# Kernel tuning notes

Hardware: AMD Instinct MI355X
Metric: run time of the kernel (lower is better)

## Reference

```python
import jax, jax.numpy as jnp
import numpy as np

N, E, D, H = 50000, 400000, 128, 256


def setup_inputs() -> dict:
    key = jax.random.key(0)
    ks = jax.random.split(key, 16)
    s = 0.02
    inp = {
        "x": jax.random.normal(ks[0], (N, D), dtype=jnp.float32),
        "edge_index": jax.random.randint(ks[1], (2, E), 0, N, dtype=jnp.int64),
        "steps": 1,
        # encoder MLP: Linear(D->H), Linear(H->H), relu after each
        "enc_w1": jax.random.normal(ks[2], (H, D), dtype=jnp.float32) * s,
        "enc_b1": jnp.zeros((H,), dtype=jnp.float32),
        "enc_w2": jax.random.normal(ks[3], (H, H), dtype=jnp.float32) * s,
        "enc_b2": jnp.zeros((H,), dtype=jnp.float32),
        # GeneralConv lin_msg (root_weight=False, bias=True)
        "msg_w": jax.random.normal(ks[4], (H, H), dtype=jnp.float32) * s,
        "msg_b": jnp.zeros((H,), dtype=jnp.float32),
        # decoder MLP: Linear(2H->H) relu, Linear(H->D) tanh
        "dec_w1": jax.random.normal(ks[5], (H, 2 * H), dtype=jnp.float32) * s,
        "dec_b1": jnp.zeros((H,), dtype=jnp.float32),
        "dec_w2": jax.random.normal(ks[6], (D, H), dtype=jnp.float32) * s,
        "dec_b2": jnp.zeros((D,), dtype=jnp.float32),
    }
    return inp


def reference(x, edge_index, steps, enc_w1, enc_b1, enc_w2, enc_b2,
              msg_w, msg_b, dec_w1, dec_b1, dec_w2, dec_b2):
    src = edge_index[0]
    dst = edge_index[1]
    n = x.shape[0]
    for _ in range(steps):  # steps is a small static python int
        # encoder MLP (batch_norm=False, dropout=0, relu + relu)
        h = jax.nn.relu(x @ enc_w1.T + enc_b1)
        h = jax.nn.relu(h @ enc_w2.T + enc_b2)
        # GeneralConv: message = lin_msg(x_j); aggr='add'; no root weight
        # lin_msg is edge-independent -> transform on nodes, then gather/scatter
        m = h @ msg_w.T + msg_b                      # [N, H]
        out = jax.ops.segment_sum(m[src], dst, num_segments=n)  # [N, H]
        # decoder on cat(out, h): relu then tanh
        d = jax.nn.relu(jnp.concatenate([out, h], axis=-1) @ dec_w1.T + dec_b1)
        x = jnp.tanh(d @ dec_w2.T + dec_b2)
    return x
```

## Files before the change

kernel.cpp:

```cpp
#include <hip/hip_runtime.h>
#include <cmath>


typedef __attribute__((ext_vector_type(8))) short  short8;
typedef __attribute__((ext_vector_type(4))) float  f32x4;
typedef __attribute__((ext_vector_type(4))) unsigned short us4;

typedef unsigned short u16;
typedef unsigned int   u32;

static __device__ __forceinline__ u16 f2bf(float f) {
    u32 u = __float_as_uint(f);
    u = (u + 0x7FFFu + ((u >> 16) & 1u)) >> 16;
    return (u16)u;
}
static __device__ __forceinline__ float bf2f(u16 h) {
    return __uint_as_float(((u32)h) << 16);
}

static __device__ __forceinline__ void g2l16(const void* g, void* l) {
    __builtin_amdgcn_global_load_lds(
        (const __attribute__((address_space(1))) u32*)g,
        (__attribute__((address_space(3))) u32*)l, 16, 0, 0);
}

__global__ __launch_bounds__(512, 4) void enc_fused(
    const float* __restrict__ x, const u16* __restrict__ w1,
    const float* __restrict__ b1, const u16* __restrict__ w2,
    const float* __restrict__ b2, const u16* __restrict__ wm,
    const float* __restrict__ bm, u16* __restrict__ hout,
    u16* __restrict__ mout, const int N)
{
    __shared__ u16 hL[8][4][512];

    const int t    = threadIdx.x;
    const int r0   = blockIdx.x * 64;
    const int wave = t >> 6;
    const int lane = t & 63;
    const int n    = lane & 15;
    const int q    = lane >> 4;
    const int wc   = wave * 32;

#pragma unroll
    for (int k = 0; k < 4; k++) {
        const int f   = t * 4 + k * 2048;
        const int row = f >> 7;
        const int col = f & 127;
        const int gr  = min(r0 + row, N - 1);
        const float4 v = *reinterpret_cast<const float4*>(
            x + (size_t)gr * 128 + col);
        us4 o = { f2bf(v.x), f2bf(v.y), f2bf(v.z), f2bf(v.w) };
        const int idx = (((col >> 3) & 3) * 16 + (row & 15)) * 8 + (col & 7);
        *reinterpret_cast<us4*>(&hL[4 + (col >> 5)][row >> 4][idx]) = o;
    }

    f32x4 acc[4][2];
#pragma unroll
    for (int i = 0; i < 4; i++)
#pragma unroll
        for (int j = 0; j < 2; j++) acc[i][j] = (f32x4)0.0f;

    short8 bp[4][2];
#pragma unroll
    for (int c = 0; c < 4; c++)
#pragma unroll
        for (int j = 0; j < 2; j++)
            bp[c][j] = *reinterpret_cast<const short8*>(
                w1 + (size_t)(wc + j * 16 + n) * 128 + c * 32 + q * 8);

    __syncthreads();

#pragma unroll
    for (int c = 0; c < 4; c++) {
        short8 af[4];
#pragma unroll
        for (int i = 0; i < 4; i++)
            af[i] = *reinterpret_cast<const short8*>(
                &hL[4 + c][i][lane * 8]);
#pragma unroll
        for (int i = 0; i < 4; i++)
#pragma unroll
            for (int j = 0; j < 2; j++)
                acc[i][j] = __builtin_amdgcn_mfma_f32_16x16x32_bf16(
                    af[i], bp[c][j], acc[i][j], 0, 0, 0);
    }

#pragma unroll
    for (int c = 0; c < 4; c++)
#pragma unroll
        for (int j = 0; j < 2; j++)
            bp[c][j] = *reinterpret_cast<const short8*>(
                w2 + (size_t)(wc + j * 16 + n) * 256 + c * 32 + q * 8);

    __syncthreads();

    {
        const float bv0 = b1[wc + n];
        const float bv1 = b1[wc + 16 + n];
        const int np = q * 4;
#pragma unroll
        for (int i = 0; i < 4; i++)
#pragma unroll
            for (int reg = 0; reg < 4; reg++) {
#pragma unroll
                for (int j = 0; j < 2; j++) {
                    const float v = fmaxf(acc[i][j][reg] + (j ? bv1 : bv0), 0.0f);
                    const int q2 = j * 2 + (n >> 3);
                    hL[wave][i][(q2 * 16 + np + reg) * 8 + (n & 7)] = f2bf(v);
                }
            }
    }
    __syncthreads();

#pragma unroll
    for (int i = 0; i < 4; i++)
#pragma unroll
        for (int j = 0; j < 2; j++) acc[i][j] = (f32x4)0.0f;
#pragma unroll
    for (int c = 0; c < 8; c++) {
        short8 af[4];
#pragma unroll
        for (int i = 0; i < 4; i++)
            af[i] = *reinterpret_cast<const short8*>(&hL[c][i][lane * 8]);
#pragma unroll
        for (int i = 0; i < 4; i++)
#pragma unroll
            for (int j = 0; j < 2; j++)
                acc[i][j] = __builtin_amdgcn_mfma_f32_16x16x32_bf16(
                    af[i], bp[c & 3][j], acc[i][j], 0, 0, 0);
        if (c < 4) {
#pragma unroll
            for (int j = 0; j < 2; j++)
                bp[c][j] = *reinterpret_cast<const short8*>(
                    w2 + (size_t)(wc + j * 16 + n) * 256 + (c + 4) * 32 + q * 8);
        }
    }

#pragma unroll
    for (int c = 0; c < 4; c++)
#pragma unroll
        for (int j = 0; j < 2; j++)
            bp[c][j] = *reinterpret_cast<const short8*>(
                wm + (size_t)(wc + j * 16 + n) * 256 + c * 32 + q * 8);

    {
        const float bv0 = b2[wc + n];
        const float bv1 = b2[wc + 16 + n];
        const int np = q * 4;
#pragma unroll
        for (int i = 0; i < 4; i++)
#pragma unroll
            for (int reg = 0; reg < 4; reg++) {
                const int row = r0 + i * 16 + q * 4 + reg;
                if (row < N) {
                    hout[(size_t)row * 256 + wc + n] =
                        f2bf(fmaxf(acc[i][0][reg] + bv0, 0.0f));
                    hout[(size_t)row * 256 + wc + 16 + n] =
                        f2bf(fmaxf(acc[i][1][reg] + bv1, 0.0f));
                }
            }
        __syncthreads();
#pragma unroll
        for (int i = 0; i < 4; i++)
#pragma unroll
            for (int reg = 0; reg < 4; reg++) {
#pragma unroll
                for (int j = 0; j < 2; j++) {
                    const float v = fmaxf(acc[i][j][reg] + (j ? bv1 : bv0), 0.0f);
                    const int q2 = j * 2 + (n >> 3);
                    hL[wave][i][(q2 * 16 + np + reg) * 8 + (n & 7)] = f2bf(v);
                }
            }
    }
    __syncthreads();

#pragma unroll
    for (int i = 0; i < 4; i++)
#pragma unroll
        for (int j = 0; j < 2; j++) acc[i][j] = (f32x4)0.0f;
#pragma unroll
    for (int c = 0; c < 8; c++) {
        short8 af[4];
#pragma unroll
        for (int i = 0; i < 4; i++)
            af[i] = *reinterpret_cast<const short8*>(&hL[c][i][lane * 8]);
#pragma unroll
        for (int i = 0; i < 4; i++)
#pragma unroll
            for (int j = 0; j < 2; j++)
                acc[i][j] = __builtin_amdgcn_mfma_f32_16x16x32_bf16(
                    af[i], bp[c & 3][j], acc[i][j], 0, 0, 0);
        if (c < 4) {
#pragma unroll
            for (int j = 0; j < 2; j++)
                bp[c][j] = *reinterpret_cast<const short8*>(
                    wm + (size_t)(wc + j * 16 + n) * 256 + (c + 4) * 32 + q * 8);
        }
    }
    {
        const float bv0 = bm[wc + n];
        const float bv1 = bm[wc + 16 + n];
#pragma unroll
        for (int i = 0; i < 4; i++)
#pragma unroll
            for (int reg = 0; reg < 4; reg++) {
                const int row = r0 + i * 16 + q * 4 + reg;
                if (row < N) {
                    mout[(size_t)row * 256 + wc + n] =
                        f2bf(acc[i][0][reg] + bv0);
                    mout[(size_t)row * 256 + wc + 16 + n] =
                        f2bf(acc[i][1][reg] + bv1);
                }
            }
    }
}

__global__ __launch_bounds__(512, 4) void dec_fused(
    const u16* __restrict__ aggr, const u16* __restrict__ h,
    const u16* __restrict__ wd1, const float* __restrict__ bd1,
    const u16* __restrict__ wd2, const float* __restrict__ bd2,
    float* __restrict__ out, const int N)
{
    __shared__ u16 dL[8][4][512];

    const int t    = threadIdx.x;
    const int r0   = blockIdx.x * 64;
    const int wave = t >> 6;
    const int lane = t & 63;
    const int n    = lane & 15;
    const int q    = lane >> 4;
    const int wc   = wave * 32;

    const int w4   = wave & 3;
    const int sub  = wave >> 2;
    const int srow = min(r0 + w4 * 16 + (lane & 15), N - 1);
    const int kq8  = (lane >> 4) * 8;
    const u16* aptr = aggr + (size_t)srow * 256 + kq8;
    const u16* hptr = h    + (size_t)srow * 256 + kq8;

#define DEC_STAGE(p, buf)                                                   \
    {                                                                       \
        const int c_  = 2 * (p) + sub;                                      \
        const int kc_ = c_ * 32;                                            \
        const u16* sp_ = (kc_ < 256) ? (aptr + kc_) : (hptr + (kc_ - 256)); \
        g2l16(sp_, &dL[(buf) * 2 + sub][w4][0]);                            \
    }

    f32x4 acc[4][2];
#pragma unroll
    for (int i = 0; i < 4; i++)
#pragma unroll
        for (int j = 0; j < 2; j++) acc[i][j] = (f32x4)0.0f;

    DEC_STAGE(0, 0);
    short8 bp[4][2];
#pragma unroll
    for (int c = 0; c < 4; c++)
#pragma unroll
        for (int j = 0; j < 2; j++)
            bp[c][j] = *reinterpret_cast<const short8*>(
                wd1 + (size_t)(wc + j * 16 + n) * 512 + c * 32 + q * 8);
    __syncthreads();

#pragma unroll
    for (int p = 0; p < 8; p++) {
        if (p < 7) DEC_STAGE(p + 1, (p + 1) & 1);
#pragma unroll
        for (int s = 0; s < 2; s++) {
            const int c = 2 * p + s;
            short8 af[4];
#pragma unroll
            for (int i = 0; i < 4; i++)
                af[i] = *reinterpret_cast<const short8*>(
                    &dL[(p & 1) * 2 + s][i][lane * 8]);
#pragma unroll
            for (int i = 0; i < 4; i++)
#pragma unroll
                for (int j = 0; j < 2; j++)
                    acc[i][j] = __builtin_amdgcn_mfma_f32_16x16x32_bf16(
                        af[i], bp[c & 3][j], acc[i][j], 0, 0, 0);
            if (c + 4 < 16) {
#pragma unroll
                for (int j = 0; j < 2; j++)
                    bp[c & 3][j] = *reinterpret_cast<const short8*>(
                        wd1 + (size_t)(wc + j * 16 + n) * 512 +
                        (c + 4) * 32 + q * 8);
            }
        }
        __syncthreads();
    }
#undef DEC_STAGE

    {
        const float bv0 = bd1[wc + n];
        const float bv1 = bd1[wc + 16 + n];
        const int np = q * 4;
#pragma unroll
        for (int i = 0; i < 4; i++)
#pragma unroll
            for (int reg = 0; reg < 4; reg++) {
#pragma unroll
                for (int j = 0; j < 2; j++) {
                    const float v = fmaxf(acc[i][j][reg] + (j ? bv1 : bv0), 0.0f);
                    const int q2 = j * 2 + (n >> 3);
                    dL[wave][i][(q2 * 16 + np + reg) * 8 + (n & 7)] = f2bf(v);
                }
            }
    }

    const int wc2 = wave * 16;
    short8 b2p[4];
#pragma unroll
    for (int c = 0; c < 4; c++)
        b2p[c] = *reinterpret_cast<const short8*>(
            wd2 + (size_t)(wc2 + n) * 256 + c * 32 + q * 8);
    __syncthreads();

    f32x4 acc2[4];
#pragma unroll
    for (int i = 0; i < 4; i++) acc2[i] = (f32x4)0.0f;
#pragma unroll
    for (int c = 0; c < 8; c++) {
        short8 af[4], bf;
#pragma unroll
        for (int i = 0; i < 4; i++)
            af[i] = *reinterpret_cast<const short8*>(&dL[c][i][lane * 8]);
        bf = b2p[c & 3];
#pragma unroll
        for (int i = 0; i < 4; i++)
            acc2[i] = __builtin_amdgcn_mfma_f32_16x16x32_bf16(
                af[i], bf, acc2[i], 0, 0, 0);
        if (c < 4)
            b2p[c] = *reinterpret_cast<const short8*>(
                wd2 + (size_t)(wc2 + n) * 256 + (c + 4) * 32 + q * 8);
    }
    {
        const float bv = bd2[wc2 + n];
#pragma unroll
        for (int i = 0; i < 4; i++)
#pragma unroll
            for (int reg = 0; reg < 4; reg++) {
                const int row = r0 + i * 16 + q * 4 + reg;
                if (row < N)
                    out[(size_t)row * 128 + wc2 + n] = tanhf(acc2[i][reg] + bv);
            }
    }
}

__global__ __launch_bounds__(256) void cvt6_kernel(
    const float* s0, const float* s1, const float* s2, const float* s3,
    const float* s4,
    u16* d0, u16* d1, u16* d2, u16* d3, u16* d4,
    int* __restrict__ zp,
    int n0, int n1, int n2, int n3, int n4, int nz)
{
    const int i = blockIdx.x * 256 + threadIdx.x;
    if (blockIdx.y == 5) {
        if (i < nz) zp[i] = 0;
        return;
    }
    const float* s; u16* d; int nq;
    switch (blockIdx.y) {
        case 0: s = s0; d = d0; nq = n0; break;
        case 1: s = s1; d = d1; nq = n1; break;
        case 2: s = s2; d = d2; nq = n2; break;
        case 3: s = s3; d = d3; nq = n3; break;
        default: s = s4; d = d4; nq = n4; break;
    }
    if (i < nq) {
        const float4 v = reinterpret_cast<const float4*>(s)[i];
        us4 o = { f2bf(v.x), f2bf(v.y), f2bf(v.z), f2bf(v.w) };
        reinterpret_cast<us4*>(d)[i] = o;
    }
}

__global__ __launch_bounds__(256) void fill_kernel(
    const int* __restrict__ ei, int* __restrict__ cursor,
    int* __restrict__ bucket, const int E, const int Nn)
{
    const int e = blockIdx.x * 256 + threadIdx.x;
    if (e < E) {
        const int src = ei[e];
        const int dst = ei[(size_t)E + e];
        if ((unsigned)dst < (unsigned)Nn) {
            const int pos = atomicAdd(&cursor[dst], 1);
            if (pos < 64) bucket[(size_t)dst * 64 + pos] = src;
        }
    }
}

__global__ __launch_bounds__(256) void gather_sum_kernel(
    const u16* __restrict__ m, const int* __restrict__ bucket,
    const int* __restrict__ cursor, u16* __restrict__ outa, const int Nn)
{
    const int wave = (int)((blockIdx.x * 256u + threadIdx.x) >> 6);
    const int lane = threadIdx.x & 63;
    if (wave >= Nn) return;
    const int cnt = min(cursor[wave], 64);
    const int* bl = bucket + (size_t)wave * 64;
    float a0 = 0.f, a1 = 0.f, a2 = 0.f, a3 = 0.f;
    for (int base = 0; base < cnt; base += 8) {
        int sidx[8];
#pragma unroll
        for (int u = 0; u < 8; u++)
            sidx[u] = (base + u < cnt) ? bl[base + u] : -1;
        us4 v[8];
#pragma unroll
        for (int u = 0; u < 8; u++) {
            const int s = ((unsigned)sidx[u] < (unsigned)Nn) ? sidx[u] : 0;
            v[u] = *reinterpret_cast<const us4*>(&m[(size_t)s * 256 + lane * 4]);
        }
#pragma unroll
        for (int u = 0; u < 8; u++) {
            if ((unsigned)sidx[u] < (unsigned)Nn) {
                a0 += bf2f(v[u].x); a1 += bf2f(v[u].y);
                a2 += bf2f(v[u].z); a3 += bf2f(v[u].w);
            }
        }
    }
    us4 o = { f2bf(a0), f2bf(a1), f2bf(a2), f2bf(a3) };
    *reinterpret_cast<us4*>(&outa[(size_t)wave * 256 + lane * 4]) = o;
}

extern "C" void kernel_launch(void* const* d_in, const int* in_sizes, int n_in,
                              void* d_out, int out_size, void* d_ws, size_t ws_size,
                              hipStream_t stream)
{
    const float* x      = (const float*)d_in[0];
    const int*   ei     = (const int*)d_in[1];
    const float* enc_w1 = (const float*)d_in[3];
    const float* enc_b1 = (const float*)d_in[4];
    const float* enc_w2 = (const float*)d_in[5];
    const float* enc_b2 = (const float*)d_in[6];
    const float* msg_w  = (const float*)d_in[7];
    const float* msg_b  = (const float*)d_in[8];
    const float* dec_w1 = (const float*)d_in[9];
    const float* dec_b1 = (const float*)d_in[10];
    const float* dec_w2 = (const float*)d_in[11];
    const float* dec_b2 = (const float*)d_in[12];

    const int N = 50000, D = 128, H = 256;
    const int E = in_sizes[1] / 2;

    u16* h    = (u16*)d_ws;
    u16* m    = h    + (size_t)N * H;
    u16* aggr = m    + (size_t)N * H;
    u16* w1   = aggr + (size_t)N * H;
    u16* w2   = w1 + 256 * 128;
    u16* wm   = w2 + 256 * 256;
    u16* wd1  = wm + 256 * 256;
    u16* wd2  = wd1 + 256 * 512;
    int* cursor = (int*)(wd2 + 128 * 256);
    int* bucket = cursor + N;

    const dim3 blk(256);
    const dim3 blk512(512);
    const int nb64 = (N + 63) / 64;
    const int cvtx = (N + 255) / 256;

    cvt6_kernel<<<dim3(cvtx, 6), blk, 0, stream>>>(
        enc_w1, enc_w2, msg_w, dec_w1, dec_w2,
        w1, w2, wm, wd1, wd2, cursor,
        256 * 128 / 4, 256 * 256 / 4, 256 * 256 / 4,
        256 * 512 / 4, 128 * 256 / 4, N);

    fill_kernel<<<dim3((E + 255) / 256), blk, 0, stream>>>(
        ei, cursor, bucket, E, N);

    enc_fused<<<dim3(nb64), blk512, 0, stream>>>(
        x, w1, enc_b1, w2, enc_b2, wm, msg_b, h, m, N);

    gather_sum_kernel<<<dim3((N * 64 + 255) / 256), blk, 0, stream>>>(
        m, bucket, cursor, aggr, N);

    dec_fused<<<dim3(nb64), blk512, 0, stream>>>(
        aggr, h, wd1, dec_b1, wd2, dec_b2, (float*)d_out, N);
}
```

Measured before the change: 255.0 us.

## Make encoder kernel persistent with register-resident weights and prefetched input tiles

The encoder kernel now launches 256 persistent blocks that loop over 64-row tiles. The w1 and w2 weight fragments are loaded into registers once per block instead of once per tile. The next tile's x rows are prefetched into registers while the current tile computes, overlapping global loads with MFMA work. This raises register pressure (launch bounds lowered to 2 blocks per CU) and cuts the grid to 256 blocks, which may underfill a GPU with many CUs and reduce latency hiding.

```diff
diff --git a/kernel.cpp b/kernel.cpp
--- a/kernel.cpp
+++ b/kernel.cpp
@@ -24,194 +24,214 @@
         (__attribute__((address_space(3))) u32*)l, 16, 0, 0);
 }
 
-__global__ __launch_bounds__(512, 4) void enc_fused(
+__global__ __launch_bounds__(512, 2) void enc_fused(
     const float* __restrict__ x, const u16* __restrict__ w1,
     const float* __restrict__ b1, const u16* __restrict__ w2,
     const float* __restrict__ b2, const u16* __restrict__ wm,
     const float* __restrict__ bm, u16* __restrict__ hout,
-    u16* __restrict__ mout, const int N)
+    u16* __restrict__ mout, const int N, const int ntiles)
 {
     __shared__ u16 hL[8][4][512];
 
     const int t    = threadIdx.x;
-    const int r0   = blockIdx.x * 64;
     const int wave = t >> 6;
     const int lane = t & 63;
     const int n    = lane & 15;
     const int q    = lane >> 4;
     const int wc   = wave * 32;
 
-#pragma unroll
-    for (int k = 0; k < 4; k++) {
-        const int f   = t * 4 + k * 2048;
-        const int row = f >> 7;
-        const int col = f & 127;
-        const int gr  = min(r0 + row, N - 1);
-        const float4 v = *reinterpret_cast<const float4*>(
-            x + (size_t)gr * 128 + col);
-        us4 o = { f2bf(v.x), f2bf(v.y), f2bf(v.z), f2bf(v.w) };
-        const int idx = (((col >> 3) & 3) * 16 + (row & 15)) * 8 + (col & 7);
-        *reinterpret_cast<us4*>(&hL[4 + (col >> 5)][row >> 4][idx]) = o;
-    }
-
-    f32x4 acc[4][2];
-#pragma unroll
-    for (int i = 0; i < 4; i++)
-#pragma unroll
-        for (int j = 0; j < 2; j++) acc[i][j] = (f32x4)0.0f;
-
-    short8 bp[4][2];
+    short8 b1f[4][2];
 #pragma unroll
     for (int c = 0; c < 4; c++)
 #pragma unroll
         for (int j = 0; j < 2; j++)
-            bp[c][j] = *reinterpret_cast<const short8*>(
+            b1f[c][j] = *reinterpret_cast<const short8*>(
                 w1 + (size_t)(wc + j * 16 + n) * 128 + c * 32 + q * 8);
-
-    __syncthreads();
-
-#pragma unroll
-    for (int c = 0; c < 4; c++) {
-        short8 af[4];
-#pragma unroll
-        for (int i = 0; i < 4; i++)
-            af[i] = *reinterpret_cast<const short8*>(
-                &hL[4 + c][i][lane * 8]);
-#pragma unroll
-        for (int i = 0; i < 4; i++)
-#pragma unroll
-            for (int j = 0; j < 2; j++)
-                acc[i][j] = __builtin_amdgcn_mfma_f32_16x16x32_bf16(
-                    af[i], bp[c][j], acc[i][j], 0, 0, 0);
-    }
-
-#pragma unroll
-    for (int c = 0; c < 4; c++)
+    short8 bW[8][2];
+#pragma unroll
+    for (int c = 0; c < 8; c++)
 #pragma unroll
         for (int j = 0; j < 2; j++)
-            bp[c][j] = *reinterpret_cast<const short8*>(
+            bW[c][j] = *reinterpret_cast<const short8*>(
                 w2 + (size_t)(wc + j * 16 + n) * 256 + c * 32 + q * 8);
-
-    __syncthreads();
-
-    {
-        const float bv0 = b1[wc + n];
-        const float bv1 = b1[wc + 16 + n];
-        const int np = q * 4;
-#pragma unroll
-        for (int i = 0; i < 4; i++)
-#pragma unroll
-            for (int reg = 0; reg < 4; reg++) {
-#pragma unroll
-                for (int j = 0; j < 2; j++) {
-                    const float v = fmaxf(acc[i][j][reg] + (j ? bv1 : bv0), 0.0f);
-                    const int q2 = j * 2 + (n >> 3);
-                    hL[wave][i][(q2 * 16 + np + reg) * 8 + (n & 7)] = f2bf(v);
-                }
-            }
-    }
-    __syncthreads();
-
-#pragma unroll
-    for (int i = 0; i < 4; i++)
-#pragma unroll
-        for (int j = 0; j < 2; j++) acc[i][j] = (f32x4)0.0f;
-#pragma unroll
-    for (int c = 0; c < 8; c++) {
-        short8 af[4];
-#pragma unroll
-        for (int i = 0; i < 4; i++)
-            af[i] = *reinterpret_cast<const short8*>(&hL[c][i][lane * 8]);
-#pragma unroll
-        for (int i = 0; i < 4; i++)
-#pragma unroll
-            for (int j = 0; j < 2; j++)
-                acc[i][j] = __builtin_amdgcn_mfma_f32_16x16x32_bf16(
-                    af[i], bp[c & 3][j], acc[i][j], 0, 0, 0);
-        if (c < 4) {
+    const float bv1_0 = b1[wc + n], bv1_1 = b1[wc + 16 + n];
+    const float bv2_0 = b2[wc + n], bv2_1 = b2[wc + 16 + n];
+    const float bvm_0 = bm[wc + n], bvm_1 = bm[wc + 16 + n];
+
+    const int xcol   = (t & 31) * 4;
+    const int xrow0  = t >> 5;
+    const int xchunk = xcol >> 5;
+    const int xidx   = (((xcol >> 3) & 3) * 16 + xrow0) * 8 + (xcol & 7);
+
+    float4 xr[4];
+    int tile = blockIdx.x;
+#pragma unroll
+    for (int kk = 0; kk < 4; kk++) {
+        const int gr = min(tile * 64 + xrow0 + kk * 16, N - 1);
+        xr[kk] = *reinterpret_cast<const float4*>(x + (size_t)gr * 128 + xcol);
+    }
+
+    for (;;) {
+        const int r0 = tile * 64;
+
+#pragma unroll
+        for (int kk = 0; kk < 4; kk++) {
+            us4 o = { f2bf(xr[kk].x), f2bf(xr[kk].y),
+                      f2bf(xr[kk].z), f2bf(xr[kk].w) };
+            *reinterpret_cast<us4*>(&hL[4 + xchunk][kk][xidx]) = o;
+        }
+        __syncthreads();
+
+        const int ntile = tile + 256;
+        if (ntile < ntiles) {
+#pragma unroll
+            for (int kk = 0; kk < 4; kk++) {
+                const int gr = min(ntile * 64 + xrow0 + kk * 16, N - 1);
+                xr[kk] = *reinterpret_cast<const float4*>(
+                    x + (size_t)gr * 128 + xcol);
+            }
+        }
+
+        f32x4 acc[4][2];
+#pragma unroll
+        for (int i = 0; i < 4; i++)
+#pragma unroll
+            for (int j = 0; j < 2; j++) acc[i][j] = (f32x4)0.0f;
+
+#pragma unroll
+        for (int c = 0; c < 4; c++) {
+            short8 af[4];
+#pragma unroll
+            for (int i = 0; i < 4; i++)
+                af[i] = *reinterpret_cast<const short8*>(
+                    &hL[4 + c][i][lane * 8]);
+#pragma unroll
+            for (int i = 0; i < 4; i++)
+#pragma unroll
+                for (int j = 0; j < 2; j++)
+                    acc[i][j] = __builtin_amdgcn_mfma_f32_16x16x32_bf16(
+                        af[i], b1f[c][j], acc[i][j], 0, 0, 0);
+        }
+
+        short8 bp[4][2];
+#pragma unroll
+        for (int c = 0; c < 4; c++)
 #pragma unroll
             for (int j = 0; j < 2; j++)
                 bp[c][j] = *reinterpret_cast<const short8*>(
-                    w2 + (size_t)(wc + j * 16 + n) * 256 + (c + 4) * 32 + q * 8);
-        }
-    }
-
-#pragma unroll
-    for (int c = 0; c < 4; c++)
-#pragma unroll
-        for (int j = 0; j < 2; j++)
-            bp[c][j] = *reinterpret_cast<const short8*>(
-                wm + (size_t)(wc + j * 16 + n) * 256 + c * 32 + q * 8);
-
-    {
-        const float bv0 = b2[wc + n];
-        const float bv1 = b2[wc + 16 + n];
-        const int np = q * 4;
-#pragma unroll
-        for (int i = 0; i < 4; i++)
-#pragma unroll
-            for (int reg = 0; reg < 4; reg++) {
-                const int row = r0 + i * 16 + q * 4 + reg;
-                if (row < N) {
-                    hout[(size_t)row * 256 + wc + n] =
-                        f2bf(fmaxf(acc[i][0][reg] + bv0, 0.0f));
-                    hout[(size_t)row * 256 + wc + 16 + n] =
-                        f2bf(fmaxf(acc[i][1][reg] + bv1, 0.0f));
+                    wm + (size_t)(wc + j * 16 + n) * 256 + c * 32 + q * 8);
+
+        __syncthreads();
+
+        {
+            const int np = q * 4;
+#pragma unroll
+            for (int i = 0; i < 4; i++)
+#pragma unroll
+                for (int reg = 0; reg < 4; reg++) {
+#pragma unroll
+                    for (int j = 0; j < 2; j++) {
+                        const float v = fmaxf(
+                            acc[i][j][reg] + (j ? bv1_1 : bv1_0), 0.0f);
+                        const int q2 = j * 2 + (n >> 3);
+                        hL[wave][i][(q2 * 16 + np + reg) * 8 + (n & 7)] =
+                            f2bf(v);
+                    }
                 }
-            }
-        __syncthreads();
-#pragma unroll
-        for (int i = 0; i < 4; i++)
-#pragma unroll
-            for (int reg = 0; reg < 4; reg++) {
-#pragma unroll
-                for (int j = 0; j < 2; j++) {
-                    const float v = fmaxf(acc[i][j][reg] + (j ? bv1 : bv0), 0.0f);
-                    const int q2 = j * 2 + (n >> 3);
-                    hL[wave][i][(q2 * 16 + np + reg) * 8 + (n & 7)] = f2bf(v);
+        }
+        __syncthreads();
+
+#pragma unroll
+        for (int i = 0; i < 4; i++)
+#pragma unroll
+            for (int j = 0; j < 2; j++) acc[i][j] = (f32x4)0.0f;
+#pragma unroll
+        for (int c = 0; c < 8; c++) {
+            short8 af[4];
+#pragma unroll
+            for (int i = 0; i < 4; i++)
+                af[i] = *reinterpret_cast<const short8*>(&hL[c][i][lane * 8]);
+#pragma unroll
+            for (int i = 0; i < 4; i++)
+#pragma unroll
+                for (int j = 0; j < 2; j++)
+                    acc[i][j] = __builtin_amdgcn_mfma_f32_16x16x32_bf16(
+                        af[i], bW[c][j], acc[i][j], 0, 0, 0);
+        }
+
+        {
+            const int np = q * 4;
+#pragma unroll
+            for (int i = 0; i < 4; i++)
+#pragma unroll
+                for (int reg = 0; reg < 4; reg++) {
+                    const int row = r0 + i * 16 + q * 4 + reg;
+                    if (row < N) {
+                        hout[(size_t)row * 256 + wc + n] =
+                            f2bf(fmaxf(acc[i][0][reg] + bv2_0, 0.0f));
+                        hout[(size_t)row * 256 + wc + 16 + n] =
+                            f2bf(fmaxf(acc[i][1][reg] + bv2_1, 0.0f));
+                    }
                 }
-            }
-    }
-    __syncthreads();
-
-#pragma unroll
-    for (int i = 0; i < 4; i++)
-#pragma unroll
-        for (int j = 0; j < 2; j++) acc[i][j] = (f32x4)0.0f;
-#pragma unroll
-    for (int c = 0; c < 8; c++) {
-        short8 af[4];
-#pragma unroll
-        for (int i = 0; i < 4; i++)
-            af[i] = *reinterpret_cast<const short8*>(&hL[c][i][lane * 8]);
-#pragma unroll
-        for (int i = 0; i < 4; i++)
-#pragma unroll
-            for (int j = 0; j < 2; j++)
-                acc[i][j] = __builtin_amdgcn_mfma_f32_16x16x32_bf16(
-                    af[i], bp[c & 3][j], acc[i][j], 0, 0, 0);
-        if (c < 4) {
-#pragma unroll
-            for (int j = 0; j < 2; j++)
-                bp[c][j] = *reinterpret_cast<const short8*>(
-                    wm + (size_t)(wc + j * 16 + n) * 256 + (c + 4) * 32 + q * 8);
-        }
-    }
-    {
-        const float bv0 = bm[wc + n];
-        const float bv1 = bm[wc + 16 + n];
-#pragma unroll
-        for (int i = 0; i < 4; i++)
-#pragma unroll
-            for (int reg = 0; reg < 4; reg++) {
-                const int row = r0 + i * 16 + q * 4 + reg;
-                if (row < N) {
-                    mout[(size_t)row * 256 + wc + n] =
-                        f2bf(acc[i][0][reg] + bv0);
-                    mout[(size_t)row * 256 + wc + 16 + n] =
-                        f2bf(acc[i][1][reg] + bv1);
+            __syncthreads();
+#pragma unroll
+            for (int i = 0; i < 4; i++)
+#pragma unroll
+                for (int reg = 0; reg < 4; reg++) {
+#pragma unroll
+                    for (int j = 0; j < 2; j++) {
+                        const float v = fmaxf(
+                            acc[i][j][reg] + (j ? bv2_1 : bv2_0), 0.0f);
+                        const int q2 = j * 2 + (n >> 3);
+                        hL[wave][i][(q2 * 16 + np + reg) * 8 + (n & 7)] =
+                            f2bf(v);
+                    }
                 }
-            }
+        }
+        __syncthreads();
+
+#pragma unroll
+        for (int i = 0; i < 4; i++)
+#pragma unroll
+            for (int j = 0; j < 2; j++) acc[i][j] = (f32x4)0.0f;
+#pragma unroll
+        for (int c = 0; c < 8; c++) {
+            short8 af[4];
+#pragma unroll
+            for (int i = 0; i < 4; i++)
+                af[i] = *reinterpret_cast<const short8*>(&hL[c][i][lane * 8]);
+#pragma unroll
+            for (int i = 0; i < 4; i++)
+#pragma unroll
+                for (int j = 0; j < 2; j++)
+                    acc[i][j] = __builtin_amdgcn_mfma_f32_16x16x32_bf16(
+                        af[i], bp[c & 3][j], acc[i][j], 0, 0, 0);
+            if (c < 4) {
+#pragma unroll
+                for (int j = 0; j < 2; j++)
+                    bp[c][j] = *reinterpret_cast<const short8*>(
+                        wm + (size_t)(wc + j * 16 + n) * 256 +
+                        (c + 4) * 32 + q * 8);
+            }
+        }
+        {
+#pragma unroll
+            for (int i = 0; i < 4; i++)
+#pragma unroll
+                for (int reg = 0; reg < 4; reg++) {
+                    const int row = r0 + i * 16 + q * 4 + reg;
+                    if (row < N) {
+                        mout[(size_t)row * 256 + wc + n] =
+                            f2bf(acc[i][0][reg] + bvm_0);
+                        mout[(size_t)row * 256 + wc + 16 + n] =
+                            f2bf(acc[i][1][reg] + bvm_1);
+                    }
+                }
+        }
+
+        tile = ntile;
+        if (tile >= ntiles) break;
+        __syncthreads();
     }
 }
 
@@ -455,7 +475,8 @@
 
     const dim3 blk(256);
     const dim3 blk512(512);
-    const int nb64 = (N + 63) / 64;
+    const int ntiles = (N + 63) / 64;
+    const int nb64 = ntiles;
     const int cvtx = (N + 255) / 256;
 
     cvt6_kernel<<<dim3(cvtx, 6), blk, 0, stream>>>(
@@ -467,8 +488,8 @@
     fill_kernel<<<dim3((E + 255) / 256), blk, 0, stream>>>(
         ei, cursor, bucket, E, N);
 
-    enc_fused<<<dim3(nb64), blk512, 0, stream>>>(
-        x, w1, enc_b1, w2, enc_b2, wm, msg_b, h, m, N);
+    enc_fused<<<dim3(256), blk512, 0, stream>>>(
+        x, w1, enc_b1, w2, enc_b2, wm, msg_b, h, m, N, ntiles);
 
     gather_sum_kernel<<<dim3((N * 64 + 255) / 256), blk, 0, stream>>>(
         m, bucket, cursor, aggr, N);
```

Result: faster. 248.8 us (-2.4%).

## Double row tile to 128 rows with 1024-thread blocks in encoder and decoder

Applied to the files above, without the earlier changes.

Both fused MLP kernels now handle 128 rows per block with 16 waves instead of 64 rows with 8 waves. Waves are split into two row halves that share the same column-slice weights, so each weight fragment loaded from global memory serves twice as many rows per block and the grid has half as many blocks. In exchange, LDS per block doubles and 1024-thread blocks with the same min-blocks hint may force register limits or lower occupancy, and the tail block wastes more rows.

```diff
diff --git a/kernel.cpp b/kernel.cpp
--- a/kernel.cpp
+++ b/kernel.cpp
@@ -24,28 +24,30 @@
         (__attribute__((address_space(3))) u32*)l, 16, 0, 0);
 }
 
-__global__ __launch_bounds__(512, 4) void enc_fused(
+__global__ __launch_bounds__(1024, 4) void enc_fused(
     const float* __restrict__ x, const u16* __restrict__ w1,
     const float* __restrict__ b1, const u16* __restrict__ w2,
     const float* __restrict__ b2, const u16* __restrict__ wm,
     const float* __restrict__ bm, u16* __restrict__ hout,
     u16* __restrict__ mout, const int N)
 {
-    __shared__ u16 hL[8][4][512];
+    __shared__ u16 hL[8][8][512];
 
     const int t    = threadIdx.x;
-    const int r0   = blockIdx.x * 64;
+    const int r0   = blockIdx.x * 128;
     const int wave = t >> 6;
     const int lane = t & 63;
     const int n    = lane & 15;
     const int q    = lane >> 4;
-    const int wc   = wave * 32;
-
-#pragma unroll
-    for (int k = 0; k < 4; k++) {
-        const int f   = t * 4 + k * 2048;
-        const int row = f >> 7;
-        const int col = f & 127;
+    const int rh   = wave >> 3;
+    const int wcw  = wave & 7;
+    const int wc   = wcw * 32;
+    const int g0   = rh * 4;
+
+#pragma unroll
+    for (int kk = 0; kk < 4; kk++) {
+        const int row = (t >> 5) + kk * 32;
+        const int col = (t & 31) * 4;
         const int gr  = min(r0 + row, N - 1);
         const float4 v = *reinterpret_cast<const float4*>(
             x + (size_t)gr * 128 + col);
@@ -76,7 +78,7 @@
 #pragma unroll
         for (int i = 0; i < 4; i++)
             af[i] = *reinterpret_cast<const short8*>(
-                &hL[4 + c][i][lane * 8]);
+                &hL[4 + c][g0 + i][lane * 8]);
 #pragma unroll
         for (int i = 0; i < 4; i++)
 #pragma unroll
@@ -106,7 +108,7 @@
                 for (int j = 0; j < 2; j++) {
                     const float v = fmaxf(acc[i][j][reg] + (j ? bv1 : bv0), 0.0f);
                     const int q2 = j * 2 + (n >> 3);
-                    hL[wave][i][(q2 * 16 + np + reg) * 8 + (n & 7)] = f2bf(v);
+                    hL[wcw][g0 + i][(q2 * 16 + np + reg) * 8 + (n & 7)] = f2bf(v);
                 }
             }
     }
@@ -121,7 +123,7 @@
         short8 af[4];
 #pragma unroll
         for (int i = 0; i < 4; i++)
-            af[i] = *reinterpret_cast<const short8*>(&hL[c][i][lane * 8]);
+            af[i] = *reinterpret_cast<const short8*>(&hL[c][g0 + i][lane * 8]);
 #pragma unroll
         for (int i = 0; i < 4; i++)
 #pragma unroll
@@ -151,7 +153,7 @@
         for (int i = 0; i < 4; i++)
 #pragma unroll
             for (int reg = 0; reg < 4; reg++) {
-                const int row = r0 + i * 16 + q * 4 + reg;
+                const int row = r0 + rh * 64 + i * 16 + q * 4 + reg;
                 if (row < N) {
                     hout[(size_t)row * 256 + wc + n] =
                         f2bf(fmaxf(acc[i][0][reg] + bv0, 0.0f));
@@ -168,7 +170,7 @@
                 for (int j = 0; j < 2; j++) {
                     const float v = fmaxf(acc[i][j][reg] + (j ? bv1 : bv0), 0.0f);
                     const int q2 = j * 2 + (n >> 3);
-                    hL[wave][i][(q2 * 16 + np + reg) * 8 + (n & 7)] = f2bf(v);
+                    hL[wcw][g0 + i][(q2 * 16 + np + reg) * 8 + (n & 7)] = f2bf(v);
                 }
             }
     }
@@ -183,7 +185,7 @@
         short8 af[4];
 #pragma unroll
         for (int i = 0; i < 4; i++)
-            af[i] = *reinterpret_cast<const short8*>(&hL[c][i][lane * 8]);
+            af[i] = *reinterpret_cast<const short8*>(&hL[c][g0 + i][lane * 8]);
 #pragma unroll
         for (int i = 0; i < 4; i++)
 #pragma unroll
@@ -204,7 +206,7 @@
         for (int i = 0; i < 4; i++)
 #pragma unroll
             for (int reg = 0; reg < 4; reg++) {
-                const int row = r0 + i * 16 + q * 4 + reg;
+                const int row = r0 + rh * 64 + i * 16 + q * 4 + reg;
                 if (row < N) {
                     mout[(size_t)row * 256 + wc + n] =
                         f2bf(acc[i][0][reg] + bv0);
@@ -215,25 +217,28 @@
     }
 }
 
-__global__ __launch_bounds__(512, 4) void dec_fused(
+__global__ __launch_bounds__(1024, 4) void dec_fused(
     const u16* __restrict__ aggr, const u16* __restrict__ h,
     const u16* __restrict__ wd1, const float* __restrict__ bd1,
     const u16* __restrict__ wd2, const float* __restrict__ bd2,
     float* __restrict__ out, const int N)
 {
-    __shared__ u16 dL[8][4][512];
+    __shared__ u16 dL[8][8][512];
 
     const int t    = threadIdx.x;
-    const int r0   = blockIdx.x * 64;
+    const int r0   = blockIdx.x * 128;
     const int wave = t >> 6;
     const int lane = t & 63;
     const int n    = lane & 15;
     const int q    = lane >> 4;
-    const int wc   = wave * 32;
-
-    const int w4   = wave & 3;
-    const int sub  = wave >> 2;
-    const int srow = min(r0 + w4 * 16 + (lane & 15), N - 1);
+    const int rh   = wave >> 3;
+    const int wcw  = wave & 7;
+    const int wc   = wcw * 32;
+    const int g0   = rh * 4;
+
+    const int sub  = wave >> 3;
+    const int w8   = wave & 7;
+    const int srow = min(r0 + w8 * 16 + (lane & 15), N - 1);
     const int kq8  = (lane >> 4) * 8;
     const u16* aptr = aggr + (size_t)srow * 256 + kq8;
     const u16* hptr = h    + (size_t)srow * 256 + kq8;
@@ -243,7 +248,7 @@
         const int c_  = 2 * (p) + sub;                                      \
         const int kc_ = c_ * 32;                                            \
         const u16* sp_ = (kc_ < 256) ? (aptr + kc_) : (hptr + (kc_ - 256)); \
-        g2l16(sp_, &dL[(buf) * 2 + sub][w4][0]);                            \
+        g2l16(sp_, &dL[(buf) * 2 + sub][w8][0]);                            \
     }
 
     f32x4 acc[4][2];
@@ -272,7 +277,7 @@
 #pragma unroll
             for (int i = 0; i < 4; i++)
                 af[i] = *reinterpret_cast<const short8*>(
-                    &dL[(p & 1) * 2 + s][i][lane * 8]);
+                    &dL[(p & 1) * 2 + s][g0 + i][lane * 8]);
 #pragma unroll
             for (int i = 0; i < 4; i++)
 #pragma unroll
@@ -303,12 +308,12 @@
                 for (int j = 0; j < 2; j++) {
                     const float v = fmaxf(acc[i][j][reg] + (j ? bv1 : bv0), 0.0f);
                     const int q2 = j * 2 + (n >> 3);
-                    dL[wave][i][(q2 * 16 + np + reg) * 8 + (n & 7)] = f2bf(v);
+                    dL[wcw][g0 + i][(q2 * 16 + np + reg) * 8 + (n & 7)] = f2bf(v);
                 }
             }
     }
 
-    const int wc2 = wave * 16;
+    const int wc2 = wcw * 16;
     short8 b2p[4];
 #pragma unroll
     for (int c = 0; c < 4; c++)
@@ -324,7 +329,7 @@
         short8 af[4], bf;
 #pragma unroll
         for (int i = 0; i < 4; i++)
-            af[i] = *reinterpret_cast<const short8*>(&dL[c][i][lane * 8]);
+            af[i] = *reinterpret_cast<const short8*>(&dL[c][g0 + i][lane * 8]);
         bf = b2p[c & 3];
 #pragma unroll
         for (int i = 0; i < 4; i++)
@@ -340,7 +345,7 @@
         for (int i = 0; i < 4; i++)
 #pragma unroll
             for (int reg = 0; reg < 4; reg++) {
-                const int row = r0 + i * 16 + q * 4 + reg;
+                const int row = r0 + rh * 64 + i * 16 + q * 4 + reg;
                 if (row < N)
                     out[(size_t)row * 128 + wc2 + n] = tanhf(acc2[i][reg] + bv);
             }
@@ -454,8 +459,8 @@
     int* bucket = cursor + N;
 
     const dim3 blk(256);
-    const dim3 blk512(512);
-    const int nb64 = (N + 63) / 64;
+    const dim3 blk1024(1024);
+    const int nb128 = (N + 127) / 128;
     const int cvtx = (N + 255) / 256;
 
     cvt6_kernel<<<dim3(cvtx, 6), blk, 0, stream>>>(
@@ -467,12 +472,12 @@
     fill_kernel<<<dim3((E + 255) / 256), blk, 0, stream>>>(
         ei, cursor, bucket, E, N);
 
-    enc_fused<<<dim3(nb64), blk512, 0, stream>>>(
+    enc_fused<<<dim3(nb128), blk1024, 0, stream>>>(
         x, w1, enc_b1, w2, enc_b2, wm, msg_b, h, m, N);
 
     gather_sum_kernel<<<dim3((N * 64 + 255) / 256), blk, 0, stream>>>(
         m, bucket, cursor, aggr, N);
 
-    dec_fused<<<dim3(nb64), blk512, 0, stream>>>(
+    dec_fused<<<dim3(nb128), blk1024, 0, stream>>>(
         aggr, h, wd1, dec_b1, wd2, dec_b2, (float*)d_out, N);
 }
```

New measurement: 262.5 us. +3.0%, slower.
